# Kernel tuning notes

Hardware: AMD Instinct MI355X
Metric: run time of the kernel (lower is better)

Reference implementation:

```python
import jax, jax.numpy as jnp
import numpy as np

B, S, D, H = 2, 4096, 768, 12
DH = D // H
SCALE = 1.0 / DH ** 0.5


def setup_inputs() -> dict:
    key = jax.random.key(0)
    k1, k2, k3, k4, k5 = jax.random.split(key, 5)
    x = jax.random.normal(k1, (B, S, D), dtype=jnp.float32)
    # nn.Linear weights: stored as [out, in]; init ~ U(-1/sqrt(in), 1/sqrt(in))
    lim = 1.0 / np.sqrt(D)
    W_qkv = jax.random.uniform(k2, (3 * D, D), minval=-lim, maxval=lim, dtype=jnp.float32)
    b_qkv = jax.random.uniform(k3, (3 * D,), minval=-lim, maxval=lim, dtype=jnp.float32)
    W_out = jax.random.uniform(k4, (D, D), minval=-lim, maxval=lim, dtype=jnp.float32)
    b_out = jax.random.uniform(k5, (D,), minval=-lim, maxval=lim, dtype=jnp.float32)
    return {"x": x, "W_qkv": W_qkv, "b_qkv": b_qkv, "W_out": W_out, "b_out": b_out}


def reference(x, W_qkv, b_qkv, W_out, b_out):
    bs, ns, _ = x.shape
    qkv = x @ W_qkv.T + b_qkv                       # [B, S, 3D]
    qkv = qkv.reshape(bs, ns, 3, H, DH)
    qkv = jnp.transpose(qkv, (2, 0, 3, 1, 4))        # [3, B, H, S, DH]
    q, k, v = qkv[0], qkv[1], qkv[2]
    attn = jnp.einsum('bhqd,bhkd->bhqk', q, k)       # [B, H, S, S]
    attn = jax.nn.softmax(attn * SCALE, axis=-1)
    out = jnp.einsum('bhqk,bhkd->bhqd', attn, v)     # [B, H, S, DH]
    out = jnp.transpose(out, (0, 2, 1, 3)).reshape(bs, ns, D)
    return out @ W_out.T + b_out
```

## Files before the change

kernel.cpp:

```cpp
#include <hip/hip_runtime.h>
#include <hip/hip_bf16.h>
#include <stdint.h>

#define B_    2
#define S_    4096
#define D_    768
#define H_    12
#define DH_   64
#define BH_   (B_*H_)
#define M_    (B_*S_)
#define NQKV_ 2304
#define QSCALE_ 0.18033688011112042f

typedef unsigned short bf16u;
typedef short bf16x8 __attribute__((ext_vector_type(8)));
typedef float f32x4 __attribute__((ext_vector_type(4)));

__device__ __forceinline__ bf16u f2bf(float f) {
    unsigned u = __float_as_uint(f);
    u += 0x7FFFu + ((u >> 16) & 1u);
    return (bf16u)(u >> 16);
}

__device__ __forceinline__ unsigned f2bf_pk(float a, float b) {
    return (unsigned)f2bf(a) | ((unsigned)f2bf(b) << 16);
}

__device__ __forceinline__ void gl_lds16(const void* g, void* l) {
    __builtin_amdgcn_global_load_lds(
        (const __attribute__((address_space(1))) unsigned*)g,
        (__attribute__((address_space(3))) unsigned*)l, 16, 0, 0);
}

#define N1Q_ 1572864
#define N2Q_  442368
#define N3Q_  147456
__global__ __launch_bounds__(256) void convert3_kernel(
    const float* __restrict__ s1, const float* __restrict__ s2,
    const float* __restrict__ s3, bf16u* __restrict__ d1,
    bf16u* __restrict__ d2, bf16u* __restrict__ d3)
{
    int i = blockIdx.x * 256 + threadIdx.x;
    const float* s; bf16u* d; int j;
    if (i < N1Q_)              { s = s1; d = d1; j = i; }
    else if (i < N1Q_ + N2Q_)  { s = s2; d = d2; j = i - N1Q_; }
    else                       { s = s3; d = d3; j = i - N1Q_ - N2Q_; }
    float4 v = ((const float4*)s)[j];
    ushort4 o;
    o.x = f2bf(v.x); o.y = f2bf(v.y); o.z = f2bf(v.z); o.w = f2bf(v.w);
    ((ushort4*)d)[j] = o;
}

template<int EPI>
__global__ __launch_bounds__(256) void gemm_kernel(
    const bf16u* __restrict__ A, const bf16u* __restrict__ Bw,
    const float* __restrict__ bias, float* __restrict__ Cout,
    bf16u* __restrict__ Qb, bf16u* __restrict__ Kb, bf16u* __restrict__ Vtb)
{
    __shared__ bf16u As[2][128*32];
    __shared__ bf16u Bs[2][128*32];
    const int tid  = threadIdx.x;
    const int lane = tid & 63;
    const int wave = tid >> 6;
    const int wr = wave >> 1, wc = wave & 1;
    const int lr = lane & 15;
    const int quad = lane >> 4;

    const int nwg  = gridDim.x * gridDim.y;
    const int fblk = blockIdx.y * gridDim.x + blockIdx.x;
    const int vblk = (fblk & 7) * (nwg >> 3) + (fblk >> 3);
    const int m0 = (vblk / gridDim.x) * 128;
    const int n0 = (vblk % gridDim.x) * 128;

    f32x4 acc[4][4];
    #pragma unroll
    for (int i = 0; i < 4; i++)
        #pragma unroll
        for (int j = 0; j < 4; j++)
            acc[i][j] = (f32x4){0.f, 0.f, 0.f, 0.f};

    auto stage = [&](int k0, int bf) {
        #pragma unroll
        for (int r = 0; r < 2; r++) {
            int c = r * 256 + tid;
            int row = c >> 2;
            int col = ((c & 3) ^ (row & 3)) * 8;
            gl_lds16(A  + (size_t)(m0 + row) * 768 + k0 + col,
                     (char*)&As[bf][0] + c * 16);
            gl_lds16(Bw + (size_t)(n0 + row) * 768 + k0 + col,
                     (char*)&Bs[bf][0] + c * 16);
        }
    };

    stage(0, 0);

    auto body = [&](int k0, int buf, bool do_stage) __attribute__((always_inline)) {
        __syncthreads();
        if (do_stage) stage(k0 + 32, buf ^ 1);
        bf16x8 af[4], bg[4];
        #pragma unroll
        for (int t = 0; t < 4; t++) {
            int ra = wr * 64 + t * 16 + lr;
            int rb = wc * 64 + t * 16 + lr;
            af[t] = *(const bf16x8*)(&As[buf][0] + ra * 32 + ((quad ^ (ra & 3)) * 8));
            bg[t] = *(const bf16x8*)(&Bs[buf][0] + rb * 32 + ((quad ^ (rb & 3)) * 8));
        }
        __builtin_amdgcn_s_setprio(1);
        #pragma unroll
        for (int i = 0; i < 4; i++)
            #pragma unroll
            for (int j = 0; j < 4; j++)
                acc[i][j] = __builtin_amdgcn_mfma_f32_16x16x32_bf16(
                    af[i], bg[j], acc[i][j], 0, 0, 0);
        __builtin_amdgcn_s_setprio(0);
    };

    #pragma unroll 1
    for (int k0 = 0; k0 < 768 - 64; k0 += 64) {
        body(k0,      0, true);
        body(k0 + 32, 1, true);
    }
    body(768 - 64, 0, true);
    body(768 - 32, 1, false);

    #pragma unroll
    for (int i = 0; i < 4; i++) {
        int mbase = m0 + wr * 64 + i * 16 + quad * 4;
        #pragma unroll
        for (int j = 0; j < 4; j++) {
            int n = n0 + wc * 64 + j * 16 + lr;
            float bv = bias[n];
            if (EPI == 0) {
                #pragma unroll
                for (int r = 0; r < 4; r++)
                    Cout[(size_t)(mbase + r) * 768 + n] = acc[i][j][r] + bv;
            } else {
                int t3  = n / 768;
                int rem = n - t3 * 768;
                int h   = rem >> 6;
                int dh  = rem & 63;
                int b   = mbase >> 12;
                int s0  = mbase & 4095;
                int bh  = b * H_ + h;
                if (t3 == 2) {
                    uint2 pk;
                    pk.x = f2bf_pk(acc[i][j][0] + bv, acc[i][j][1] + bv);
                    pk.y = f2bf_pk(acc[i][j][2] + bv, acc[i][j][3] + bv);
                    *(uint2*)(Vtb + ((size_t)bh * DH_ + dh) * S_ + s0) = pk;
                } else if (t3 == 0) {
                    #pragma unroll
                    for (int r = 0; r < 4; r++)
                        Qb[((size_t)bh * S_ + s0 + r) * DH_ + dh] =
                            f2bf((acc[i][j][r] + bv) * QSCALE_);
                } else {
                    #pragma unroll
                    for (int r = 0; r < 4; r++)
                        Kb[((size_t)bh * S_ + s0 + r) * DH_ + dh] =
                            f2bf(acc[i][j][r] + bv);
                }
            }
        }
    }
}

__global__ __launch_bounds__(512, 4) void attn_kernel(
    const bf16u* __restrict__ Qb, const bf16u* __restrict__ Kb,
    const bf16u* __restrict__ Vtb, bf16u* __restrict__ A2)
{
    __shared__ char Lds[33280];
    const int tid  = threadIdx.x;
    const int lane = tid & 63;
    const int w    = tid >> 6;
    const int grp  = w >> 2;
    const int wq   = (w & 3) * 32;
    const int lr   = lane & 15;
    const int quad = lane >> 4;

    const int fblk = blockIdx.y * gridDim.x + blockIdx.x;
    const int vblk = (fblk & 7) * 96 + (fblk >> 3);
    const int q0   = (vblk & 31) * 128;
    const int bh   = vblk >> 5;

    const size_t kbase_g = (size_t)bh * S_ * DH_;
    const size_t vbase_g = (size_t)bh * DH_ * S_;

    bf16x8 aq[2][2];
    #pragma unroll
    for (int rh = 0; rh < 2; rh++) {
        const size_t qb = ((size_t)bh * S_ + q0 + wq + rh * 16 + lr) * DH_ + quad * 8;
        aq[rh][0] = *(const bf16x8*)(Qb + qb);
        aq[rh][1] = *(const bf16x8*)(Qb + qb + 32);
    }

    bf16x8 onesf;
    #pragma unroll
    for (int j = 0; j < 8; j++) onesf[j] = (short)0x3F80;

    f32x4 o[2][4];
    f32x4 l_acc[2];
    #pragma unroll
    for (int rh = 0; rh < 2; rh++) {
        l_acc[rh] = (f32x4){0.f, 0.f, 0.f, 0.f};
        #pragma unroll
        for (int t = 0; t < 4; t++) o[rh][t] = (f32x4){0.f, 0.f, 0.f, 0.f};
    }

    int kaddr[2][2];
    #pragma unroll
    for (int ntk = 0; ntk < 2; ntk++) {
        int rk = ntk * 16 + lr;
        kaddr[ntk][0] = rk * 128 + ((quad ^ (rk & 7)) * 16);
        kaddr[ntk][1] = rk * 128 + (((4 + quad) ^ (rk & 7)) * 16);
    }
    int vaddr[4];
    #pragma unroll
    for (int nt = 0; nt < 4; nt++) {
        int rv = nt * 16 + lr;
        int sr = rv >> 1;
        int slot = ((rv & 1) << 2) | quad;
        vaddr[nt] = sr * 128 + ((slot ^ (sr & 7)) * 16);
    }

    auto stage = [&](int u, int pp) {
        const int g  = tid >> 8;
        const int c  = tid & 255;
        const int kv0 = g * (S_ / 2) + u * 32;
        int krow = c >> 3;
        int kcol = ((c & 7) ^ (krow & 7)) * 8;
        gl_lds16(Kb + kbase_g + (size_t)(kv0 + krow) * DH_ + kcol,
                 Lds + pp * 8192 + g * 4096 + c * 16);
        int sr = c >> 3;
        int lslot = (c & 7) ^ (sr & 7);
        int dh  = sr * 2 + (lslot >> 2);
        int kvc = (lslot & 3) * 8;
        gl_lds16(Vtb + vbase_g + (size_t)dh * S_ + kv0 + kvc,
                 Lds + 16384 + pp * 8192 + g * 4096 + c * 16);
    };

    stage(0, 0);

    auto body = [&](int u, int pp, bool do_stage) __attribute__((always_inline)) {
        __syncthreads();
        if (do_stage) stage(u + 1, pp ^ 1);

        const char* Kbuf = Lds + pp * 8192 + grp * 4096;
        const char* Vbuf = Lds + 16384 + pp * 8192 + grp * 4096;

        f32x4 sc[2][2];
        __builtin_amdgcn_s_setprio(1);
        #pragma unroll
        for (int ntk = 0; ntk < 2; ntk++) {
            const bf16x8 bk0 = *(const bf16x8*)(Kbuf + kaddr[ntk][0]);
            const bf16x8 bk1 = *(const bf16x8*)(Kbuf + kaddr[ntk][1]);
            #pragma unroll
            for (int rh = 0; rh < 2; rh++) {
                f32x4 s = (f32x4){0.f, 0.f, 0.f, 0.f};
                s = __builtin_amdgcn_mfma_f32_16x16x32_bf16(bk0, aq[rh][0], s, 0, 0, 0);
                s = __builtin_amdgcn_mfma_f32_16x16x32_bf16(bk1, aq[rh][1], s, 0, 0, 0);
                sc[rh][ntk] = s;
            }
        }
        __builtin_amdgcn_s_setprio(0);

        unsigned W[2][2][2];
        #pragma unroll
        for (int rh = 0; rh < 2; rh++) {
            #pragma unroll
            for (int ntk = 0; ntk < 2; ntk++) {
                float p0 = __builtin_amdgcn_exp2f(sc[rh][ntk][0]);
                float p1 = __builtin_amdgcn_exp2f(sc[rh][ntk][1]);
                float p2 = __builtin_amdgcn_exp2f(sc[rh][ntk][2]);
                float p3 = __builtin_amdgcn_exp2f(sc[rh][ntk][3]);
                W[rh][ntk][0] = __builtin_amdgcn_perm(__float_as_uint(p1),
                                                      __float_as_uint(p0), 0x07060302u);
                W[rh][ntk][1] = __builtin_amdgcn_perm(__float_as_uint(p3),
                                                      __float_as_uint(p2), 0x07060302u);
            }
        }

        bf16x8 ap[2];
        #pragma unroll
        for (int rh = 0; rh < 2; rh++) {
            union { unsigned u4[4]; bf16x8 v; } Af;
            #pragma unroll
            for (int b = 0; b < 2; b++) {
                auto r1 = __builtin_amdgcn_permlane32_swap(
                    W[rh][0][b], W[rh][1][b], false, false);
                auto r2 = __builtin_amdgcn_permlane16_swap(
                    r1[0], r1[1], false, false);
                Af.u4[b]     = r2[0];
                Af.u4[2 + b] = r2[1];
            }
            ap[rh] = Af.v;
        }

        __builtin_amdgcn_s_setprio(1);
        #pragma unroll
        for (int rh = 0; rh < 2; rh++)
            l_acc[rh] = __builtin_amdgcn_mfma_f32_16x16x32_bf16(ap[rh], onesf, l_acc[rh], 0, 0, 0);
        #pragma unroll
        for (int nt = 0; nt < 4; nt++) {
            const bf16x8 bv = *(const bf16x8*)(Vbuf + vaddr[nt]);
            #pragma unroll
            for (int rh = 0; rh < 2; rh++)
                o[rh][nt] = __builtin_amdgcn_mfma_f32_16x16x32_bf16(ap[rh], bv, o[rh][nt], 0, 0, 0);
        }
        __builtin_amdgcn_s_setprio(0);
    };

    #pragma unroll 1
    for (int u = 0; u < 62; u += 2) {
        body(u,     0, true);
        body(u + 1, 1, true);
    }
    body(62, 0, true);
    body(63, 1, false);

    __syncthreads();
    float* LO = (float*)Lds;
    float* LL = (float*)(Lds + 32768);
    if (grp == 0) {
        #pragma unroll
        for (int rh = 0; rh < 2; rh++) {
            #pragma unroll
            for (int r2 = 0; r2 < 4; r2++)
                LL[wq + rh * 16 + quad * 4 + r2] = l_acc[rh][r2];
            #pragma unroll
            for (int nt = 0; nt < 4; nt++)
                #pragma unroll
                for (int r2 = 0; r2 < 4; r2++)
                    LO[(wq + rh * 16 + quad * 4 + r2) * 64 + nt * 16 + lr] =
                        o[rh][nt][r2];
        }
    }
    __syncthreads();
    if (grp == 1) {
        const int b = bh / H_, h = bh % H_;
        #pragma unroll
        for (int rh = 0; rh < 2; rh++) {
            float rl[4];
            #pragma unroll
            for (int r2 = 0; r2 < 4; r2++)
                rl[r2] = 1.0f / (l_acc[rh][r2] + LL[wq + rh * 16 + quad * 4 + r2]);
            #pragma unroll
            for (int nt = 0; nt < 4; nt++)
                #pragma unroll
                for (int r2 = 0; r2 < 4; r2++) {
                    int row = wq + rh * 16 + quad * 4 + r2;
                    int q = q0 + row;
                    float v = (o[rh][nt][r2] + LO[row * 64 + nt * 16 + lr]) * rl[r2];
                    A2[((size_t)b * S_ + q) * D_ + h * DH_ + nt * 16 + lr] = f2bf(v);
                }
        }
    }
}

extern "C" void kernel_launch(void* const* d_in, const int* in_sizes, int n_in,
                              void* d_out, int out_size, void* d_ws, size_t ws_size,
                              hipStream_t stream) {
    const float* x     = (const float*)d_in[0];
    const float* W_qkv = (const float*)d_in[1];
    const float* b_qkv = (const float*)d_in[2];
    const float* W_out = (const float*)d_in[3];
    const float* b_out = (const float*)d_in[4];
    float* out = (float*)d_out;
    char* ws = (char*)d_ws;

    bf16u* xb    = (bf16u*)(ws + 0);
    bf16u* wqkvb = (bf16u*)(ws + 12582912);
    bf16u* woutb = (bf16u*)(ws + 16121856);
    bf16u* Qb    = (bf16u*)(ws + 17301504);
    bf16u* Kb    = (bf16u*)(ws + 29884416);
    bf16u* Vtb   = (bf16u*)(ws + 42467328);
    bf16u* A2    = (bf16u*)(ws + 55050240);

    convert3_kernel<<<(N1Q_ + N2Q_ + N3Q_) / 256, 256, 0, stream>>>(
        x, W_qkv, W_out, xb, wqkvb, woutb);

    dim3 g1(NQKV_/128, M_/128);
    gemm_kernel<1><<<g1, 256, 0, stream>>>(xb, wqkvb, b_qkv, nullptr, Qb, Kb, Vtb);

    dim3 g2(S_/128, BH_);
    attn_kernel<<<g2, 512, 0, stream>>>(Qb, Kb, Vtb, A2);

    dim3 g3(D_/128, M_/128);
    gemm_kernel<0><<<g3, 256, 0, stream>>>(A2, woutb, b_out, out, nullptr, nullptr, nullptr);
}
```

Before: 252.6 us.

## Software-pipeline attention loop with triple-buffered K/V and QK lookahead

The attention inner loop is restructured so the QK^T MFMAs for tile u+1 are issued alongside the softmax and PV work for tile u. K/V staging moves from double to triple buffering with a prefetch distance of two tiles, and there is one barrier per iteration instead of a barrier before each stage. The aim is to hide exp/permute latency and LDS waits behind matrix work. In exchange, LDS per block grows to 48 KB and more score registers stay live, which may cut how many blocks fit on each CU.

```diff
diff --git a/kernel.cpp b/kernel.cpp
--- a/kernel.cpp
+++ b/kernel.cpp
@@ -167,7 +167,7 @@
     const bf16u* __restrict__ Qb, const bf16u* __restrict__ Kb,
     const bf16u* __restrict__ Vtb, bf16u* __restrict__ A2)
 {
-    __shared__ char Lds[33280];
+    __shared__ char Lds[49152];
     const int tid  = threadIdx.x;
     const int lane = tid & 63;
     const int w    = tid >> 6;
@@ -221,33 +221,26 @@
         vaddr[nt] = sr * 128 + ((slot ^ (sr & 7)) * 16);
     }
 
-    auto stage = [&](int u, int pp) {
+    auto stage = [&](int u, int b) {
         const int g  = tid >> 8;
         const int c  = tid & 255;
         const int kv0 = g * (S_ / 2) + u * 32;
         int krow = c >> 3;
         int kcol = ((c & 7) ^ (krow & 7)) * 8;
         gl_lds16(Kb + kbase_g + (size_t)(kv0 + krow) * DH_ + kcol,
-                 Lds + pp * 8192 + g * 4096 + c * 16);
+                 Lds + b * 8192 + g * 4096 + c * 16);
         int sr = c >> 3;
         int lslot = (c & 7) ^ (sr & 7);
         int dh  = sr * 2 + (lslot >> 2);
         int kvc = (lslot & 3) * 8;
         gl_lds16(Vtb + vbase_g + (size_t)dh * S_ + kv0 + kvc,
-                 Lds + 16384 + pp * 8192 + g * 4096 + c * 16);
-    };
-
-    stage(0, 0);
-
-    auto body = [&](int u, int pp, bool do_stage) __attribute__((always_inline)) {
-        __syncthreads();
-        if (do_stage) stage(u + 1, pp ^ 1);
-
-        const char* Kbuf = Lds + pp * 8192 + grp * 4096;
-        const char* Vbuf = Lds + 16384 + pp * 8192 + grp * 4096;
-
-        f32x4 sc[2][2];
-        __builtin_amdgcn_s_setprio(1);
+                 Lds + 24576 + b * 8192 + g * 4096 + c * 16);
+    };
+
+    f32x4 sc[2][2];
+
+    auto qk_tile = [&](f32x4 (&scD)[2][2], int bK) __attribute__((always_inline)) {
+        const char* Kbuf = Lds + bK * 8192 + grp * 4096;
         #pragma unroll
         for (int ntk = 0; ntk < 2; ntk++) {
             const bf16x8 bk0 = *(const bf16x8*)(Kbuf + kaddr[ntk][0]);
@@ -257,35 +250,32 @@
                 f32x4 s = (f32x4){0.f, 0.f, 0.f, 0.f};
                 s = __builtin_amdgcn_mfma_f32_16x16x32_bf16(bk0, aq[rh][0], s, 0, 0, 0);
                 s = __builtin_amdgcn_mfma_f32_16x16x32_bf16(bk1, aq[rh][1], s, 0, 0, 0);
-                sc[rh][ntk] = s;
+                scD[rh][ntk] = s;
             }
         }
-        __builtin_amdgcn_s_setprio(0);
-
-        unsigned W[2][2][2];
+    };
+
+    auto sm_pv = [&](int bV) __attribute__((always_inline)) {
+        bf16x8 ap[2];
         #pragma unroll
         for (int rh = 0; rh < 2; rh++) {
+            unsigned W[2][2];
             #pragma unroll
             for (int ntk = 0; ntk < 2; ntk++) {
                 float p0 = __builtin_amdgcn_exp2f(sc[rh][ntk][0]);
                 float p1 = __builtin_amdgcn_exp2f(sc[rh][ntk][1]);
                 float p2 = __builtin_amdgcn_exp2f(sc[rh][ntk][2]);
                 float p3 = __builtin_amdgcn_exp2f(sc[rh][ntk][3]);
-                W[rh][ntk][0] = __builtin_amdgcn_perm(__float_as_uint(p1),
-                                                      __float_as_uint(p0), 0x07060302u);
-                W[rh][ntk][1] = __builtin_amdgcn_perm(__float_as_uint(p3),
-                                                      __float_as_uint(p2), 0x07060302u);
+                W[ntk][0] = __builtin_amdgcn_perm(__float_as_uint(p1),
+                                                  __float_as_uint(p0), 0x07060302u);
+                W[ntk][1] = __builtin_amdgcn_perm(__float_as_uint(p3),
+                                                  __float_as_uint(p2), 0x07060302u);
             }
-        }
-
-        bf16x8 ap[2];
-        #pragma unroll
-        for (int rh = 0; rh < 2; rh++) {
             union { unsigned u4[4]; bf16x8 v; } Af;
             #pragma unroll
             for (int b = 0; b < 2; b++) {
                 auto r1 = __builtin_amdgcn_permlane32_swap(
-                    W[rh][0][b], W[rh][1][b], false, false);
+                    W[0][b], W[1][b], false, false);
                 auto r2 = __builtin_amdgcn_permlane16_swap(
                     r1[0], r1[1], false, false);
                 Af.u4[b]     = r2[0];
@@ -293,7 +283,7 @@
             }
             ap[rh] = Af.v;
         }
-
+        const char* Vbuf = Lds + 24576 + bV * 8192 + grp * 4096;
         __builtin_amdgcn_s_setprio(1);
         #pragma unroll
         for (int rh = 0; rh < 2; rh++)
@@ -308,13 +298,35 @@
         __builtin_amdgcn_s_setprio(0);
     };
 
+    auto body = [&](int u, int bK, int bV, int bst, bool do_stage)
+        __attribute__((always_inline)) {
+        if (do_stage) stage(u + 2, bst);
+        f32x4 scN[2][2];
+        qk_tile(scN, bK);
+        sm_pv(bV);
+        #pragma unroll
+        for (int i = 0; i < 2; i++)
+            #pragma unroll
+            for (int j = 0; j < 2; j++)
+                sc[i][j] = scN[i][j];
+        __syncthreads();
+    };
+
+    stage(0, 0);
+    stage(1, 1);
+    __syncthreads();
+    qk_tile(sc, 0);
+
     #pragma unroll 1
-    for (int u = 0; u < 62; u += 2) {
-        body(u,     0, true);
-        body(u + 1, 1, true);
-    }
-    body(62, 0, true);
-    body(63, 1, false);
+    for (int u = 0; u < 60; u += 3) {
+        body(u,     1, 0, 2, true);
+        body(u + 1, 2, 1, 0, true);
+        body(u + 2, 0, 2, 1, true);
+    }
+    body(60, 1, 0, 2, true);
+    body(61, 2, 1, 0, true);
+    body(62, 0, 2, 1, false);
+    sm_pv(0);
 
     __syncthreads();
     float* LO = (float*)Lds;
```

New measurement: 256.4 us. Within noise of the previous version (+1.5%).
